# Optimization experiments

Hardware: AMD Instinct MI355X
Metric: run time of the kernel (lower is better)

Reference implementation:

```python
import jax, jax.numpy as jnp
import numpy as np

# --- configuration (matches init_kwargs) ---
K = 8            # number of cluster fields
L = 8            # hashgrid levels
T = 2 ** 18      # hash table size per level (log2_hashmap_size=18)
F = 2            # features per level
HID = 64         # MLP hidden dim
BASE_RES = 16    # base resolution; max_res=2048 -> growth factor 2
N_PTS = 524288

PRIMES = np.array([1, 2654435761, 805459861], dtype=np.uint32)
RES = (BASE_RES * 2 ** np.arange(L)).astype(np.float32)  # [16,32,...,2048]
CORNERS = np.array([[i, j, k] for i in (0, 1) for j in (0, 1) for k in (0, 1)],
                   dtype=np.float32)  # [8,3] trilinear corner offsets


def setup_inputs() -> dict:
    key = jax.random.key(0)
    ks = jax.random.split(key, 6)
    return {
        "positions": jax.random.uniform(ks[0], (N_PTS, 3), dtype=jnp.float32),
        "centroids": jax.random.uniform(ks[1], (K, 3), dtype=jnp.float32),
        "tables":    jax.random.normal(ks[2], (K, L, T, F), dtype=jnp.float32) * 1e-2,
        "W1":        jax.random.normal(ks[3], (K, L * F, HID), dtype=jnp.float32) * 0.1,
        "b1":        jnp.zeros((K, HID), dtype=jnp.float32),
        "W2":        jax.random.normal(ks[4], (K, HID, 1), dtype=jnp.float32) * 0.1,
        "b2":        jnp.zeros((K, 1), dtype=jnp.float32),
    }


def _hash_encode(positions, tables, assign):
    """Multi-resolution hash encoding, table selected per-point by cluster assignment."""
    N = positions.shape[0]
    res = jnp.asarray(RES)                                    # [L]
    scaled = positions[:, None, :] * res[None, :, None]       # [N,L,3]
    f = jnp.floor(scaled)
    w = scaled - f                                            # [N,L,3] trilinear fracs
    corners = jnp.asarray(CORNERS)                            # [8,3]
    ci = (f[:, :, None, :] + corners[None, None]).astype(jnp.uint32)  # [N,L,8,3]
    p = jnp.asarray(PRIMES)
    h = (ci[..., 0] * p[0]) ^ (ci[..., 1] * p[1]) ^ (ci[..., 2] * p[2])
    h = (h & jnp.uint32(T - 1)).astype(jnp.int32)             # [N,L,8]
    lvl = jnp.arange(L, dtype=jnp.int32)
    # flat index into [K*L*T, F] table selects the assigned field's grid
    flat = (assign[:, None, None] * L + lvl[None, :, None]) * T + h   # [N,L,8]
    feats = tables.reshape(K * L * T, F)[flat]                # [N,L,8,F] gather
    cw = jnp.prod(jnp.where(corners[None, None] > 0.5,
                            w[:, :, None, :], 1.0 - w[:, :, None, :]), axis=-1)  # [N,L,8]
    enc = jnp.sum(feats * cw[..., None], axis=2)              # [N,L,F]
    return enc.reshape(N, L * F)


def reference(positions, centroids, tables, W1, b1, W2, b2):
    # cdist + argmin cluster routing
    d2 = jnp.sum((positions[:, None, :] - centroids[None]) ** 2, axis=-1)  # [N,K]
    assign = jnp.argmin(d2, axis=1).astype(jnp.int32)                      # [N]
    enc = _hash_encode(positions, tables, assign)                          # [N, L*F]
    dens = jnp.zeros((positions.shape[0], 1), dtype=positions.dtype)
    for k in range(K):  # small fixed loop over structurally distinct fields
        h = jax.nn.relu(enc @ W1[k] + b1[k])
        dk = jnp.exp(h @ W2[k] + b2[k])  # trunc_exp density activation
        dens = jnp.where((assign == k)[:, None], dk, dens)
    return dens  # [N,1]
```

## Files before the change

### kernel.cpp

```cpp
#include <hip/hip_runtime.h>
#include <math.h>

#define KF 8
#define LL 8
#define TT (1 << 18)
#define FF 2
#define HID 64
#define INF 16
#define W1S 1056
#define BS  68

__global__ __launch_bounds__(256) void propnet_density_kernel(
    const float* __restrict__ positions,
    const float* __restrict__ centroids,
    const float* __restrict__ tables,
    const float* __restrict__ W1,
    const float* __restrict__ b1,
    const float* __restrict__ W2,
    const float* __restrict__ b2,
    float* __restrict__ out,
    int npts)
{
    __shared__ float sW1[KF * W1S];
    __shared__ float sB1[KF * BS];
    __shared__ float sW2[KF * BS];
    __shared__ float sB2[KF];
    __shared__ float sC[KF * 3];

    const int tid = threadIdx.x;

    for (int idx = tid; idx < KF * INF * HID; idx += blockDim.x) {
        int k = idx >> 10;
        int r = idx & 1023;
        sW1[k * W1S + r] = W1[idx];
    }
    for (int idx = tid; idx < KF * HID; idx += blockDim.x) {
        int k = idx >> 6;
        int r = idx & 63;
        sB1[k * BS + r] = b1[idx];
        sW2[k * BS + r] = W2[idx];
    }
    if (tid < KF) sB2[tid] = b2[tid];
    if (tid < KF * 3) sC[tid] = centroids[tid];
    __syncthreads();

    const int gid = blockIdx.x * blockDim.x + tid;
    if (gid >= npts) return;

    const float px = positions[gid * 3 + 0];
    const float py = positions[gid * 3 + 1];
    const float pz = positions[gid * 3 + 2];

    int assign = 0;
    float best = 1e30f;
    #pragma unroll
    for (int k = 0; k < KF; ++k) {
        float dx = px - sC[k * 3 + 0];
        float dy = py - sC[k * 3 + 1];
        float dz = pz - sC[k * 3 + 2];
        float d2 = fmaf(dx, dx, fmaf(dy, dy, dz * dz));
        bool lt = d2 < best;
        assign = lt ? k : assign;
        best = lt ? d2 : best;
    }

    float enc[INF];
    const float2* __restrict__ tab =
        (const float2*)tables + (size_t)assign * (LL * (size_t)TT);

    #pragma unroll
    for (int l = 0; l < LL; ++l) {
        const float res = (float)(16 << l);
        const float sx = px * res, sy = py * res, sz = pz * res;
        const float fx = floorf(sx), fy = floorf(sy), fz = floorf(sz);
        const float wx = sx - fx, wy = sy - fy, wz = sz - fz;
        const unsigned ix = (unsigned)(int)fx;
        const unsigned iy = (unsigned)(int)fy;
        const unsigned iz = (unsigned)(int)fz;

        const float2* __restrict__ tl = tab + (size_t)l * TT;

        const unsigned hx0 = ix;
        const unsigned hx1 = ix + 1u;
        const unsigned hy0 = iy * 2654435761u;
        const unsigned hy1 = (iy + 1u) * 2654435761u;
        const unsigned hz0 = iz * 805459861u;
        const unsigned hz1 = (iz + 1u) * 805459861u;
        const unsigned M = TT - 1;

        const float2 c000 = tl[(hx0 ^ hy0 ^ hz0) & M];
        const float2 c001 = tl[(hx0 ^ hy0 ^ hz1) & M];
        const float2 c010 = tl[(hx0 ^ hy1 ^ hz0) & M];
        const float2 c011 = tl[(hx0 ^ hy1 ^ hz1) & M];
        const float2 c100 = tl[(hx1 ^ hy0 ^ hz0) & M];
        const float2 c101 = tl[(hx1 ^ hy0 ^ hz1) & M];
        const float2 c110 = tl[(hx1 ^ hy1 ^ hz0) & M];
        const float2 c111 = tl[(hx1 ^ hy1 ^ hz1) & M];

        const float ux = 1.f - wx, uy = 1.f - wy, uz = 1.f - wz;
        const float w000 = ux * uy * uz, w001 = ux * uy * wz;
        const float w010 = ux * wy * uz, w011 = ux * wy * wz;
        const float w100 = wx * uy * uz, w101 = wx * uy * wz;
        const float w110 = wx * wy * uz, w111 = wx * wy * wz;

        enc[l * 2 + 0] = c000.x * w000 + c001.x * w001 + c010.x * w010 + c011.x * w011
                       + c100.x * w100 + c101.x * w101 + c110.x * w110 + c111.x * w111;
        enc[l * 2 + 1] = c000.y * w000 + c001.y * w001 + c010.y * w010 + c011.y * w011
                       + c100.y * w100 + c101.y * w101 + c110.y * w110 + c111.y * w111;
    }

    const float4* __restrict__ w1k = (const float4*)(sW1 + assign * W1S);
    const float4* __restrict__ b1k = (const float4*)(sB1 + assign * BS);
    const float4* __restrict__ w2k = (const float4*)(sW2 + assign * BS);

    float outv = sB2[assign];
    #pragma unroll
    for (int j4 = 0; j4 < HID / 4; ++j4) {
        float4 a = b1k[j4];
        #pragma unroll
        for (int i = 0; i < INF; ++i) {
            const float4 w = w1k[i * (HID / 4) + j4];
            const float e = enc[i];
            a.x = fmaf(e, w.x, a.x);
            a.y = fmaf(e, w.y, a.y);
            a.z = fmaf(e, w.z, a.z);
            a.w = fmaf(e, w.w, a.w);
        }
        a.x = fmaxf(a.x, 0.f); a.y = fmaxf(a.y, 0.f);
        a.z = fmaxf(a.z, 0.f); a.w = fmaxf(a.w, 0.f);
        const float4 w2v = w2k[j4];
        outv = fmaf(a.x, w2v.x, outv);
        outv = fmaf(a.y, w2v.y, outv);
        outv = fmaf(a.z, w2v.z, outv);
        outv = fmaf(a.w, w2v.w, outv);
    }

    out[gid] = expf(outv);
}

extern "C" void kernel_launch(void* const* d_in, const int* in_sizes, int n_in,
                              void* d_out, int out_size, void* d_ws, size_t ws_size,
                              hipStream_t stream) {
    const float* positions = (const float*)d_in[0];
    const float* centroids = (const float*)d_in[1];
    const float* tables    = (const float*)d_in[2];
    const float* W1        = (const float*)d_in[3];
    const float* b1        = (const float*)d_in[4];
    const float* W2        = (const float*)d_in[5];
    const float* b2        = (const float*)d_in[6];
    float* out = (float*)d_out;

    const int npts = in_sizes[0] / 3;
    const int block = 256;
    const int grid = (npts + block - 1) / block;

    propnet_density_kernel<<<grid, block, 0, stream>>>(
        positions, centroids, tables, W1, b1, W2, b2, out, npts);
}
```

Measured before the change: 424.3 us.

## Sort points by cluster and split gather per level for table cache locality

Replaces the single fused kernel with a pipeline. The pipeline counts cluster assignments, scans them, and scatters points into cluster-sorted order in workspace. A separate gather kernel then processes one (cluster, level) table slice per block group, so each 2 MB table slice stays hot in cache. An MLP kernel reads the stored encodings and writes results back to the original indices. This trades several extra launches and extra global traffic (sorted positions plus an N×16 float encoding buffer) for better cache reuse in the random hash-table gathers. A fused fallback is kept for when the workspace is too small.

```diff
diff --git a/kernel.cpp b/kernel.cpp
--- a/kernel.cpp
+++ b/kernel.cpp
@@ -4,23 +4,154 @@
 #define KF 8
 #define LL 8
 #define TT (1 << 18)
-#define FF 2
 #define HID 64
 #define INF 16
-#define W1S 1056
-#define BS  68
-
-__global__ __launch_bounds__(256) void propnet_density_kernel(
-    const float* __restrict__ positions,
-    const float* __restrict__ centroids,
-    const float* __restrict__ tables,
-    const float* __restrict__ W1,
-    const float* __restrict__ b1,
-    const float* __restrict__ W2,
-    const float* __restrict__ b2,
-    float* __restrict__ out,
-    int npts)
-{
+#define W1S 1064
+#define BS  72
+#define BT  256
+#define CCH 256
+
+
+__device__ __forceinline__ int cluster_assign(float px, float py, float pz,
+                                              const float* __restrict__ c) {
+    int a = 0; float best = 1e30f;
+    #pragma unroll
+    for (int k = 0; k < KF; ++k) {
+        float dx = px - c[k * 3 + 0];
+        float dy = py - c[k * 3 + 1];
+        float dz = pz - c[k * 3 + 2];
+        float d2 = fmaf(dx, dx, fmaf(dy, dy, dz * dz));
+        bool lt = d2 < best;
+        a = lt ? k : a;
+        best = lt ? d2 : best;
+    }
+    return a;
+}
+
+__device__ __forceinline__ float2 gather_level(const float2* __restrict__ tl,
+                                               float px, float py, float pz, int l) {
+    const float res = (float)(16 << l);
+    const float sx = px * res, sy = py * res, sz = pz * res;
+    const float fx = floorf(sx), fy = floorf(sy), fz = floorf(sz);
+    const float wx = sx - fx, wy = sy - fy, wz = sz - fz;
+    const unsigned ix = (unsigned)(int)fx;
+    const unsigned iy = (unsigned)(int)fy;
+    const unsigned iz = (unsigned)(int)fz;
+
+    const unsigned hx0 = ix;
+    const unsigned hx1 = ix + 1u;
+    const unsigned hy0 = iy * 2654435761u;
+    const unsigned hy1 = (iy + 1u) * 2654435761u;
+    const unsigned hz0 = iz * 805459861u;
+    const unsigned hz1 = (iz + 1u) * 805459861u;
+    const unsigned M = TT - 1;
+
+    const float2 c000 = tl[(hx0 ^ hy0 ^ hz0) & M];
+    const float2 c001 = tl[(hx0 ^ hy0 ^ hz1) & M];
+    const float2 c010 = tl[(hx0 ^ hy1 ^ hz0) & M];
+    const float2 c011 = tl[(hx0 ^ hy1 ^ hz1) & M];
+    const float2 c100 = tl[(hx1 ^ hy0 ^ hz0) & M];
+    const float2 c101 = tl[(hx1 ^ hy0 ^ hz1) & M];
+    const float2 c110 = tl[(hx1 ^ hy1 ^ hz0) & M];
+    const float2 c111 = tl[(hx1 ^ hy1 ^ hz1) & M];
+
+    const float ux = 1.f - wx, uy = 1.f - wy, uz = 1.f - wz;
+    const float w000 = ux * uy * uz, w001 = ux * uy * wz;
+    const float w010 = ux * wy * uz, w011 = ux * wy * wz;
+    const float w100 = wx * uy * uz, w101 = wx * uy * wz;
+    const float w110 = wx * wy * uz, w111 = wx * wy * wz;
+
+    float ex = c000.x * w000 + c001.x * w001 + c010.x * w010 + c011.x * w011
+             + c100.x * w100 + c101.x * w101 + c110.x * w110 + c111.x * w111;
+    float ey = c000.y * w000 + c001.y * w001 + c010.y * w010 + c011.y * w011
+             + c100.y * w100 + c101.y * w101 + c110.y * w110 + c111.y * w111;
+    return make_float2(ex, ey);
+}
+
+
+__global__ void k_init(int* p) {
+    if (threadIdx.x < 16) p[threadIdx.x] = 0;
+}
+
+__global__ __launch_bounds__(BT) void k_count(const float* __restrict__ pos,
+                                              const float* __restrict__ cent,
+                                              int* __restrict__ counts, int n) {
+    __shared__ int h[KF];
+    if (threadIdx.x < KF) h[threadIdx.x] = 0;
+    __syncthreads();
+    const int gid = blockIdx.x * BT + threadIdx.x;
+    if (gid < n) {
+        float px = pos[gid * 3], py = pos[gid * 3 + 1], pz = pos[gid * 3 + 2];
+        atomicAdd(&h[cluster_assign(px, py, pz, cent)], 1);
+    }
+    __syncthreads();
+    if (threadIdx.x < KF && h[threadIdx.x] > 0)
+        atomicAdd(&counts[threadIdx.x], h[threadIdx.x]);
+}
+
+__global__ void k_scan(const int* __restrict__ counts,
+                       int* __restrict__ base, int* __restrict__ cursor) {
+    if (threadIdx.x == 0) {
+        int acc = 0;
+        for (int k = 0; k < KF; ++k) { base[k] = acc; cursor[k] = acc; acc += counts[k]; }
+    }
+}
+
+__global__ __launch_bounds__(BT) void k_scatter(const float* __restrict__ pos,
+                                                const float* __restrict__ cent,
+                                                int* __restrict__ cursor,
+                                                float4* __restrict__ sorted, int n) {
+    __shared__ int h[KF];
+    __shared__ int gb[KF];
+    if (threadIdx.x < KF) h[threadIdx.x] = 0;
+    __syncthreads();
+    const int gid = blockIdx.x * BT + threadIdx.x;
+    int a = 0, r = 0;
+    float px = 0.f, py = 0.f, pz = 0.f;
+    if (gid < n) {
+        px = pos[gid * 3]; py = pos[gid * 3 + 1]; pz = pos[gid * 3 + 2];
+        a = cluster_assign(px, py, pz, cent);
+        r = atomicAdd(&h[a], 1);
+    }
+    __syncthreads();
+    if (threadIdx.x < KF && h[threadIdx.x] > 0)
+        gb[threadIdx.x] = atomicAdd(&cursor[threadIdx.x], h[threadIdx.x]);
+    __syncthreads();
+    if (gid < n)
+        sorted[gb[a] + r] = make_float4(px, py, pz, __int_as_float(gid));
+}
+
+
+__global__ __launch_bounds__(BT, 8) void k_gather(const float2* __restrict__ tables,
+                                                  const float4* __restrict__ sorted,
+                                                  const int* __restrict__ base,
+                                                  const int* __restrict__ counts,
+                                                  float2* __restrict__ enc, int n) {
+    const int b = blockIdx.x;
+    const int k = b & 7;
+    const int t = b >> 3;
+    const int c = t & (CCH - 1);
+    const int l = t >> 8;
+    const int start = base[k];
+    const int cnt = counts[k];
+    const float2* __restrict__ tl = tables + ((size_t)k * LL + l) * TT;
+    float2* __restrict__ encl = enc + (size_t)l * n;
+
+    for (int i = c * BT + threadIdx.x; i < cnt; i += CCH * BT) {
+        const float4 p = sorted[start + i];
+        encl[start + i] = gather_level(tl, p.x, p.y, p.z, l);
+    }
+}
+
+
+__global__ __launch_bounds__(BT) void k_mlp(const float4* __restrict__ sorted,
+                                            const float2* __restrict__ enc,
+                                            const float* __restrict__ cent,
+                                            const float* __restrict__ W1,
+                                            const float* __restrict__ b1,
+                                            const float* __restrict__ W2,
+                                            const float* __restrict__ b2,
+                                            float* __restrict__ out, int n) {
     __shared__ float sW1[KF * W1S];
     __shared__ float sB1[KF * BS];
     __shared__ float sW2[KF * BS];
@@ -28,85 +159,33 @@
     __shared__ float sC[KF * 3];
 
     const int tid = threadIdx.x;
-
-    for (int idx = tid; idx < KF * INF * HID; idx += blockDim.x) {
+    for (int idx = tid; idx < KF * INF * HID; idx += BT) {
         int k = idx >> 10;
         int r = idx & 1023;
         sW1[k * W1S + r] = W1[idx];
     }
-    for (int idx = tid; idx < KF * HID; idx += blockDim.x) {
+    for (int idx = tid; idx < KF * HID; idx += BT) {
         int k = idx >> 6;
         int r = idx & 63;
         sB1[k * BS + r] = b1[idx];
         sW2[k * BS + r] = W2[idx];
     }
     if (tid < KF) sB2[tid] = b2[tid];
-    if (tid < KF * 3) sC[tid] = centroids[tid];
-    __syncthreads();
-
-    const int gid = blockIdx.x * blockDim.x + tid;
-    if (gid >= npts) return;
-
-    const float px = positions[gid * 3 + 0];
-    const float py = positions[gid * 3 + 1];
-    const float pz = positions[gid * 3 + 2];
-
-    int assign = 0;
-    float best = 1e30f;
-    #pragma unroll
-    for (int k = 0; k < KF; ++k) {
-        float dx = px - sC[k * 3 + 0];
-        float dy = py - sC[k * 3 + 1];
-        float dz = pz - sC[k * 3 + 2];
-        float d2 = fmaf(dx, dx, fmaf(dy, dy, dz * dz));
-        bool lt = d2 < best;
-        assign = lt ? k : assign;
-        best = lt ? d2 : best;
-    }
-
-    float enc[INF];
-    const float2* __restrict__ tab =
-        (const float2*)tables + (size_t)assign * (LL * (size_t)TT);
-
+    if (tid < KF * 3) sC[tid] = cent[tid];
+    __syncthreads();
+
+    const int gid = blockIdx.x * BT + tid;
+    if (gid >= n) return;
+
+    const float4 p = sorted[gid];
+    const int assign = cluster_assign(p.x, p.y, p.z, sC);
+
+    float encr[INF];
     #pragma unroll
     for (int l = 0; l < LL; ++l) {
-        const float res = (float)(16 << l);
-        const float sx = px * res, sy = py * res, sz = pz * res;
-        const float fx = floorf(sx), fy = floorf(sy), fz = floorf(sz);
-        const float wx = sx - fx, wy = sy - fy, wz = sz - fz;
-        const unsigned ix = (unsigned)(int)fx;
-        const unsigned iy = (unsigned)(int)fy;
-        const unsigned iz = (unsigned)(int)fz;
-
-        const float2* __restrict__ tl = tab + (size_t)l * TT;
-
-        const unsigned hx0 = ix;
-        const unsigned hx1 = ix + 1u;
-        const unsigned hy0 = iy * 2654435761u;
-        const unsigned hy1 = (iy + 1u) * 2654435761u;
-        const unsigned hz0 = iz * 805459861u;
-        const unsigned hz1 = (iz + 1u) * 805459861u;
-        const unsigned M = TT - 1;
-
-        const float2 c000 = tl[(hx0 ^ hy0 ^ hz0) & M];
-        const float2 c001 = tl[(hx0 ^ hy0 ^ hz1) & M];
-        const float2 c010 = tl[(hx0 ^ hy1 ^ hz0) & M];
-        const float2 c011 = tl[(hx0 ^ hy1 ^ hz1) & M];
-        const float2 c100 = tl[(hx1 ^ hy0 ^ hz0) & M];
-        const float2 c101 = tl[(hx1 ^ hy0 ^ hz1) & M];
-        const float2 c110 = tl[(hx1 ^ hy1 ^ hz0) & M];
-        const float2 c111 = tl[(hx1 ^ hy1 ^ hz1) & M];
-
-        const float ux = 1.f - wx, uy = 1.f - wy, uz = 1.f - wz;
-        const float w000 = ux * uy * uz, w001 = ux * uy * wz;
-        const float w010 = ux * wy * uz, w011 = ux * wy * wz;
-        const float w100 = wx * uy * uz, w101 = wx * uy * wz;
-        const float w110 = wx * wy * uz, w111 = wx * wy * wz;
-
-        enc[l * 2 + 0] = c000.x * w000 + c001.x * w001 + c010.x * w010 + c011.x * w011
-                       + c100.x * w100 + c101.x * w101 + c110.x * w110 + c111.x * w111;
-        enc[l * 2 + 1] = c000.y * w000 + c001.y * w001 + c010.y * w010 + c011.y * w011
-                       + c100.y * w100 + c101.y * w101 + c110.y * w110 + c111.y * w111;
+        const float2 e = enc[(size_t)l * n + gid];
+        encr[l * 2 + 0] = e.x;
+        encr[l * 2 + 1] = e.y;
     }
 
     const float4* __restrict__ w1k = (const float4*)(sW1 + assign * W1S);
@@ -120,7 +199,7 @@
         #pragma unroll
         for (int i = 0; i < INF; ++i) {
             const float4 w = w1k[i * (HID / 4) + j4];
-            const float e = enc[i];
+            const float e = encr[i];
             a.x = fmaf(e, w.x, a.x);
             a.y = fmaf(e, w.y, a.y);
             a.z = fmaf(e, w.z, a.z);
@@ -135,8 +214,84 @@
         outv = fmaf(a.w, w2v.w, outv);
     }
 
+    out[__float_as_int(p.w)] = expf(outv);
+}
+
+
+__global__ __launch_bounds__(BT) void k_fused(const float* __restrict__ positions,
+                                              const float* __restrict__ centroids,
+                                              const float* __restrict__ tables,
+                                              const float* __restrict__ W1,
+                                              const float* __restrict__ b1,
+                                              const float* __restrict__ W2,
+                                              const float* __restrict__ b2,
+                                              float* __restrict__ out, int npts) {
+    __shared__ float sW1[KF * W1S];
+    __shared__ float sB1[KF * BS];
+    __shared__ float sW2[KF * BS];
+    __shared__ float sB2[KF];
+    __shared__ float sC[KF * 3];
+
+    const int tid = threadIdx.x;
+    for (int idx = tid; idx < KF * INF * HID; idx += BT) {
+        int k = idx >> 10; int r = idx & 1023;
+        sW1[k * W1S + r] = W1[idx];
+    }
+    for (int idx = tid; idx < KF * HID; idx += BT) {
+        int k = idx >> 6; int r = idx & 63;
+        sB1[k * BS + r] = b1[idx];
+        sW2[k * BS + r] = W2[idx];
+    }
+    if (tid < KF) sB2[tid] = b2[tid];
+    if (tid < KF * 3) sC[tid] = centroids[tid];
+    __syncthreads();
+
+    const int gid = blockIdx.x * BT + tid;
+    if (gid >= npts) return;
+
+    const float px = positions[gid * 3 + 0];
+    const float py = positions[gid * 3 + 1];
+    const float pz = positions[gid * 3 + 2];
+    const int assign = cluster_assign(px, py, pz, sC);
+
+    float encr[INF];
+    const float2* __restrict__ tab =
+        (const float2*)tables + (size_t)assign * (LL * (size_t)TT);
+    #pragma unroll
+    for (int l = 0; l < LL; ++l) {
+        float2 e = gather_level(tab + (size_t)l * TT, px, py, pz, l);
+        encr[l * 2 + 0] = e.x;
+        encr[l * 2 + 1] = e.y;
+    }
+
+    const float4* __restrict__ w1k = (const float4*)(sW1 + assign * W1S);
+    const float4* __restrict__ b1k = (const float4*)(sB1 + assign * BS);
+    const float4* __restrict__ w2k = (const float4*)(sW2 + assign * BS);
+
+    float outv = sB2[assign];
+    #pragma unroll
+    for (int j4 = 0; j4 < HID / 4; ++j4) {
+        float4 a = b1k[j4];
+        #pragma unroll
+        for (int i = 0; i < INF; ++i) {
+            const float4 w = w1k[i * (HID / 4) + j4];
+            const float e = encr[i];
+            a.x = fmaf(e, w.x, a.x);
+            a.y = fmaf(e, w.y, a.y);
+            a.z = fmaf(e, w.z, a.z);
+            a.w = fmaf(e, w.w, a.w);
+        }
+        a.x = fmaxf(a.x, 0.f); a.y = fmaxf(a.y, 0.f);
+        a.z = fmaxf(a.z, 0.f); a.w = fmaxf(a.w, 0.f);
+        const float4 w2v = w2k[j4];
+        outv = fmaf(a.x, w2v.x, outv);
+        outv = fmaf(a.y, w2v.y, outv);
+        outv = fmaf(a.z, w2v.z, outv);
+        outv = fmaf(a.w, w2v.w, outv);
+    }
     out[gid] = expf(outv);
 }
+
 
 extern "C" void kernel_launch(void* const* d_in, const int* in_sizes, int n_in,
                               void* d_out, int out_size, void* d_ws, size_t ws_size,
@@ -150,10 +305,29 @@
     const float* b2        = (const float*)d_in[6];
     float* out = (float*)d_out;
 
-    const int npts = in_sizes[0] / 3;
-    const int block = 256;
-    const int grid = (npts + block - 1) / block;
-
-    propnet_density_kernel<<<grid, block, 0, stream>>>(
-        positions, centroids, tables, W1, b1, W2, b2, out, npts);
-}
+    const int n = in_sizes[0] / 3;
+    const int nblk = (n + BT - 1) / BT;
+
+    const size_t need = 256 + (size_t)n * 16 + (size_t)LL * n * 8;
+
+    if (ws_size >= need) {
+        char* ws = (char*)d_ws;
+        int* counts   = (int*)(ws + 0);
+        int* base     = (int*)(ws + 64);
+        int* cursor   = (int*)(ws + 128);
+        float4* sorted = (float4*)(ws + 256);
+        float2* enc    = (float2*)(ws + 256 + (size_t)n * 16);
+
+        k_init<<<1, 64, 0, stream>>>(counts);
+        k_count<<<nblk, BT, 0, stream>>>(positions, centroids, counts, n);
+        k_scan<<<1, 64, 0, stream>>>(counts, base, cursor);
+        k_scatter<<<nblk, BT, 0, stream>>>(positions, centroids, cursor, sorted, n);
+        k_gather<<<LL * CCH * KF, BT, 0, stream>>>((const float2*)tables, sorted,
+                                                   base, counts, enc, n);
+        k_mlp<<<nblk, BT, 0, stream>>>(sorted, enc, centroids,
+                                       W1, b1, W2, b2, out, n);
+    } else {
+        k_fused<<<nblk, BT, 0, stream>>>(positions, centroids, tables,
+                                         W1, b1, W2, b2, out, n);
+    }
+}
```

Result: slower. 467.0 us (+10.1%).
